# Optimization experiments

Measured on AMD Instinct MI355X. Metric: run time of the kernel, lower is better.

The kernel has to match this reference:

```python
import jax, jax.numpy as jnp
import numpy as np

N_NODES = 50000
N_EDGES = 1_600_000
IN_C, HID_C, OUT_C = 512, 256, 50
ALPHA = 0.1
NUM_LAYERS = 10


def setup_inputs() -> dict:
    key = jax.random.key(0)
    ks = jax.random.split(key, 8)
    x = jax.random.normal(ks[0], (N_NODES, IN_C), dtype=jnp.float32)
    edge_row = jax.random.randint(ks[1], (N_EDGES,), 0, N_NODES, dtype=jnp.int32)
    edge_col = jax.random.randint(ks[2], (N_EDGES,), 0, N_NODES, dtype=jnp.int32)
    edge_weight = jax.random.uniform(ks[3], (N_EDGES,), dtype=jnp.float32)
    s1 = 1.0 / np.sqrt(IN_C)
    s2 = 1.0 / np.sqrt(HID_C)
    W1 = jax.random.uniform(ks[4], (IN_C, HID_C), minval=-s1, maxval=s1, dtype=jnp.float32)
    b1 = jax.random.uniform(ks[5], (HID_C,), minval=-s1, maxval=s1, dtype=jnp.float32)
    W2 = jax.random.uniform(ks[6], (HID_C, OUT_C), minval=-s2, maxval=s2, dtype=jnp.float32)
    b2 = jax.random.uniform(ks[7], (OUT_C,), minval=-s2, maxval=s2, dtype=jnp.float32)
    return {"x": x, "edge_row": edge_row, "edge_col": edge_col,
            "edge_weight": edge_weight, "W1": W1, "b1": b1, "W2": W2, "b2": b2}


def reference(x, edge_row, edge_col, edge_weight, W1, b1, W2, b2):
    # MLP: Linear -> ReLU -> Linear (dropout inactive in eval, no batch norm)
    h = jax.nn.relu(x @ W1 + b1)          # [N, HID_C]
    h = h @ W2 + b2                        # [N, OUT_C]
    x0 = h

    def spmm(v):
        # out[i] = sum_{e: row[e]==i} w[e] * v[col[e]]
        msgs = v[edge_col] * edge_weight[:, None]   # [E, OUT_C]
        return jax.ops.segment_sum(msgs, edge_row, num_segments=N_NODES)

    def step(h, _):
        h = spmm(h) * (1.0 - ALPHA) + ALPHA * x0
        return h, None

    h, _ = jax.lax.scan(step, h, None, length=NUM_LAYERS)
    return jax.nn.log_softmax(h, axis=1)
```

## Files before the change

kernel.cpp:

```cpp
#include <hip/hip_runtime.h>
#include <cstddef>
#include <cstdint>
#include <math.h>

#define N_NODES 50000
#define N_EDGES 1600000
#define IN_C 512
#define HID_C 256
#define OUT_C 50
#define PAD_C 64
#define NUM_LAYERS 10
#define NBUCK 98
#define BSHIFT 9
#define BCAP 20480
#define PHB_CHUNK 8192
#define PHB_BLOCKS 196

typedef __attribute__((ext_vector_type(8))) short short8;
typedef __attribute__((ext_vector_type(4))) float floatx4;

__device__ inline unsigned short f2bf(float f) {
    unsigned int u = __float_as_uint(f);
    u += 0x7fffu + ((u >> 16) & 1u);
    return (unsigned short)(u >> 16);
}

__device__ inline unsigned cvtpk(float lo, float hi) {
    unsigned r;
    asm("v_cvt_pk_bf16_f32 %0, %1, %2" : "=v"(r) : "v"(lo), "v"(hi));
    return r;
}

__device__ inline short8 pack_bf16x8(float4 lo, float4 hi) {
    union { unsigned u[4]; short8 s; } r;
    r.u[0] = cvtpk(lo.x, lo.y);
    r.u[1] = cvtpk(lo.z, lo.w);
    r.u[2] = cvtpk(hi.x, hi.y);
    r.u[3] = cvtpk(hi.z, hi.w);
    return r.s;
}

#define ASYNC16(g, l)                                                     \
    __builtin_amdgcn_global_load_lds(                                     \
        (const __attribute__((address_space(1))) void*)(g),               \
        (__attribute__((address_space(3))) void*)(l), 16, 0, 0)

__global__ __launch_bounds__(256) void transpose_w1(const float* __restrict__ W1,
                                                    unsigned short* __restrict__ Wt) {
    __shared__ float tile[32][33];
    int bx = blockIdx.x;
    int by = blockIdx.y;
    int tx = threadIdx.x & 31, ty = threadIdx.x >> 5;
#pragma unroll
    for (int i = 0; i < 32; i += 8)
        tile[ty + i][tx] = W1[(bx * 32 + ty + i) * HID_C + by * 32 + tx];
    __syncthreads();
#pragma unroll
    for (int i = 0; i < 32; i += 8)
        Wt[(size_t)(by * 32 + ty + i) * IN_C + bx * 32 + tx] = f2bf(tile[tx][ty + i]);
}

__global__ void pad_w2(const float* __restrict__ W2, const float* __restrict__ b2,
                       unsigned short* __restrict__ Wpt, float* __restrict__ bp) {
    int idx = blockIdx.x * blockDim.x + threadIdx.x;
    if (idx < PAD_C * HID_C) {
        int n = idx >> 8, k = idx & 255;
        float v = (n < OUT_C) ? W2[k * OUT_C + n] : 0.f;
        Wpt[idx] = f2bf(v);
    }
    if (idx < PAD_C) bp[idx] = (idx < OUT_C) ? b2[idx] : 0.f;
}

__global__ __launch_bounds__(256) void gemm1_fused(const float* __restrict__ A,
                                                   const unsigned short* __restrict__ Wt,
                                                   const float* __restrict__ b1,
                                                   const unsigned short* __restrict__ Wpt,
                                                   const float* __restrict__ bp,
                                                   float* __restrict__ h0f,
                                                   unsigned short* __restrict__ h0b) {
    __shared__ __align__(16) char smem[33792];
    unsigned short* Bs0 = (unsigned short*)smem;
    unsigned short* Bs1 = (unsigned short*)(smem + 16384);
    unsigned short* Hs  = (unsigned short*)smem;
    const int HS_LD = 264;

    const int tid  = threadIdx.x;
    const int wave = tid >> 6, lane = tid & 63;
    const int quad = lane >> 4, l16 = lane & 15;
    const int m0 = blockIdx.x * 64;
    const int wm = (wave >> 1) * 32;
    const int wn = (wave & 1) * 128;

    floatx4 acc[2][8];
#pragma unroll
    for (int i = 0; i < 2; ++i)
#pragma unroll
        for (int j = 0; j < 8; ++j) acc[i][j] = (floatx4){0.f, 0.f, 0.f, 0.f};

    int r0 = m0 + wm + l16;
    int r1 = r0 + 16;
    if (r0 >= N_NODES) r0 = N_NODES - 1;
    if (r1 >= N_NODES) r1 = N_NODES - 1;
    const float* a0 = A + (size_t)r0 * IN_C + (quad << 3);
    const float* a1 = A + (size_t)r1 * IN_C + (quad << 3);

    auto stageB = [&](unsigned short* Bs_, int k0) {
#pragma unroll
        for (int j = 0; j < 4; ++j) {
            const unsigned short* src = Wt + (size_t)tid * IN_C + k0 + (j << 3);
            ASYNC16(src, Bs_ + (j << 11) + (tid << 3));
        }
    };

    float4 pa[4];
    auto loadA = [&](int k0) {
        pa[0] = *(const float4*)(a0 + k0);
        pa[1] = *(const float4*)(a0 + k0 + 4);
        pa[2] = *(const float4*)(a1 + k0);
        pa[3] = *(const float4*)(a1 + k0 + 4);
    };

    auto compute = [&](const unsigned short* Bs_, short8 af0, short8 af1) {
#pragma unroll
        for (int nt = 0; nt < 8; ++nt) {
            short8 bf = *(const short8*)&Bs_[(quad << 11) + ((wn + nt * 16 + l16) << 3)];
            acc[0][nt] = __builtin_amdgcn_mfma_f32_16x16x32_bf16(af0, bf, acc[0][nt], 0, 0, 0);
            acc[1][nt] = __builtin_amdgcn_mfma_f32_16x16x32_bf16(af1, bf, acc[1][nt], 0, 0, 0);
        }
    };

    stageB(Bs0, 0);
    loadA(0);
    __syncthreads();

    for (int kp = 0; kp < 8; ++kp) {
        const int k0 = kp * 64;
        stageB(Bs1, k0 + 32);
        {
            short8 af0 = pack_bf16x8(pa[0], pa[1]);
            short8 af1 = pack_bf16x8(pa[2], pa[3]);
            loadA(k0 + 32);
            compute(Bs0, af0, af1);
        }
        __syncthreads();
        if (kp < 7) stageB(Bs0, k0 + 64);
        {
            short8 af0 = pack_bf16x8(pa[0], pa[1]);
            short8 af1 = pack_bf16x8(pa[2], pa[3]);
            if (kp < 7) loadA(k0 + 64);
            compute(Bs1, af0, af1);
        }
        __syncthreads();
    }

#pragma unroll
    for (int nt = 0; nt < 8; ++nt) {
        int n = wn + nt * 16 + l16;
        float bn = b1[n];
#pragma unroll
        for (int mt = 0; mt < 2; ++mt)
#pragma unroll
            for (int r = 0; r < 4; ++r) {
                float v = acc[mt][nt][r] + bn;
                v = v > 0.f ? v : 0.f;
                Hs[(wm + mt * 16 + quad * 4 + r) * HS_LD + n] = f2bf(v);
            }
    }
    __syncthreads();

    floatx4 acc2[4];
#pragma unroll
    for (int nt = 0; nt < 4; ++nt) acc2[nt] = (floatx4){0.f, 0.f, 0.f, 0.f};
    const int hrow = (wave << 4) + l16;
#pragma unroll
    for (int k2 = 0; k2 < 8; ++k2) {
        short8 haf = *(const short8*)&Hs[hrow * HS_LD + (k2 << 5) + (quad << 3)];
#pragma unroll
        for (int nt = 0; nt < 4; ++nt) {
            short8 bf = *(const short8*)&Wpt[(size_t)((nt << 4) + l16) * HID_C + (k2 << 5) + (quad << 3)];
            acc2[nt] = __builtin_amdgcn_mfma_f32_16x16x32_bf16(haf, bf, acc2[nt], 0, 0, 0);
        }
    }
#pragma unroll
    for (int nt = 0; nt < 4; ++nt) {
        int c = (nt << 4) + l16;
        float bn = bp[c];
#pragma unroll
        for (int r = 0; r < 4; ++r) {
            int row = m0 + (wave << 4) + (quad << 2) + r;
            if (row < N_NODES) {
                float v = acc2[nt][r] + bn;
                h0f[(size_t)row * PAD_C + c] = v;
                h0b[(size_t)row * PAD_C + c] = f2bf(v);
            }
        }
    }
}

__global__ __launch_bounds__(256) void bucket_scatter(const int* __restrict__ erow,
                                                      const int* __restrict__ ecol,
                                                      const float* __restrict__ ew,
                                                      int* __restrict__ bfill,
                                                      uint2* __restrict__ buckets) {
    __shared__ int lcnt[NBUCK];
    __shared__ int lbase[NBUCK];
    const int t = threadIdx.x;
    for (int b = t; b < NBUCK; b += 256) lcnt[b] = 0;
    __syncthreads();
    const int e0 = blockIdx.x * PHB_CHUNK;
    const int e1 = min(e0 + PHB_CHUNK, N_EDGES);
    for (int e = e0 + t; e < e1; e += 256)
        atomicAdd(&lcnt[erow[e] >> BSHIFT], 1);
    __syncthreads();
    for (int b = t; b < NBUCK; b += 256) {
        lbase[b] = atomicAdd(&bfill[b], lcnt[b]);
        lcnt[b] = 0;
    }
    __syncthreads();
    for (int e = e0 + t; e < e1; e += 256) {
        int r = erow[e];
        int b = r >> BSHIFT;
        int o = atomicAdd(&lcnt[b], 1);
        int idx = lbase[b] + o;
        if (idx < BCAP) {
            unsigned packed = ((unsigned)(r - (b << BSHIFT)) << 17) | (unsigned)ecol[e];
            buckets[(size_t)b * BCAP + idx] = make_uint2(packed, __float_as_uint(ew[e]));
        }
    }
}

__global__ __launch_bounds__(128) void bucket_scan(const int* __restrict__ bfill,
                                                   int* __restrict__ bbase,
                                                   int* __restrict__ rowptr) {
    __shared__ int sd[128];
    int t = threadIdx.x;
    int v = (t < NBUCK) ? min(bfill[t], BCAP) : 0;
    sd[t] = v;
    __syncthreads();
    for (int off = 1; off < 128; off <<= 1) {
        int x = (t >= off) ? sd[t - off] : 0;
        __syncthreads();
        sd[t] += x;
        __syncthreads();
    }
    if (t < NBUCK) bbase[t] = sd[t] - v;
    if (t == NBUCK - 1) {
        bbase[NBUCK] = sd[t];
        rowptr[N_NODES] = sd[t];
    }
}

__global__ __launch_bounds__(256) void bucket_csr(const uint2* __restrict__ buckets,
                                                  const int* __restrict__ bfill,
                                                  const int* __restrict__ bbase,
                                                  int* __restrict__ rowptr,
                                                  uint2* __restrict__ edges) {
    __shared__ int hist[512];
    __shared__ int excl[512];
    __shared__ int psum[256];
    const int b = blockIdx.x;
    const int t = threadIdx.x;
    const int n = min(bfill[b], BCAP);
    const uint2* bk = buckets + (size_t)b * BCAP;

    hist[t] = 0; hist[t + 256] = 0;
    __syncthreads();
    for (int i = t; i < n; i += 256)
        atomicAdd(&hist[bk[i].x >> 17], 1);
    __syncthreads();
    int a0 = hist[2 * t], a1 = hist[2 * t + 1];
    psum[t] = a0 + a1;
    __syncthreads();
    for (int off = 1; off < 256; off <<= 1) {
        int x = (t >= off) ? psum[t - off] : 0;
        __syncthreads();
        psum[t] += x;
        __syncthreads();
    }
    int pe = psum[t] - (a0 + a1);
    excl[2 * t] = pe;
    excl[2 * t + 1] = pe + a0;
    __syncthreads();
    const int base = bbase[b];
#pragma unroll
    for (int k = 0; k < 2; ++k) {
        int lr = t + k * 256;
        int r = (b << BSHIFT) + lr;
        if (r < N_NODES) rowptr[r] = base + excl[lr];
    }
    hist[t] = 0; hist[t + 256] = 0;
    __syncthreads();
    for (int i = t; i < n; i += 256) {
        uint2 ed = bk[i];
        int lr = ed.x >> 17;
        int pos = base + excl[lr] + atomicAdd(&hist[lr], 1);
        edges[pos] = make_uint2(ed.x & 0x1FFFFu, ed.y);
    }
}

__device__ inline void edge_fma(float* acc, float wgt, uint4 hv) {
    acc[0] = fmaf(wgt, __uint_as_float(hv.x << 16),         acc[0]);
    acc[1] = fmaf(wgt, __uint_as_float(hv.x & 0xffff0000u), acc[1]);
    acc[2] = fmaf(wgt, __uint_as_float(hv.y << 16),         acc[2]);
    acc[3] = fmaf(wgt, __uint_as_float(hv.y & 0xffff0000u), acc[3]);
    acc[4] = fmaf(wgt, __uint_as_float(hv.z << 16),         acc[4]);
    acc[5] = fmaf(wgt, __uint_as_float(hv.z & 0xffff0000u), acc[5]);
    acc[6] = fmaf(wgt, __uint_as_float(hv.w << 16),         acc[6]);
    acc[7] = fmaf(wgt, __uint_as_float(hv.w & 0xffff0000u), acc[7]);
}

template <bool LAST>
__global__ __launch_bounds__(256) void prop8(const int* __restrict__ rowptr,
                                             const uint2* __restrict__ edges,
                                             const unsigned short* __restrict__ hin,
                                             const float* __restrict__ h0f,
                                             unsigned short* __restrict__ hout_b,
                                             float* __restrict__ out_f) {
    int wid = (blockIdx.x * blockDim.x + threadIdx.x) >> 6;
    if (wid >= N_NODES) return;
    int lane = threadIdx.x & 63;
    int slot = lane >> 3;
    int lc   = lane & 7;
    int s = rowptr[wid], e = rowptr[wid + 1];

    float acc0[8], acc1[8];
#pragma unroll
    for (int k = 0; k < 8; ++k) { acc0[k] = 0.f; acc1[k] = 0.f; }

    int i = s;
    for (; i + 32 <= e; i += 32) {
        uint2 cw0 = edges[i + slot];
        uint2 cw1 = edges[i + 8 + slot];
        uint2 cw2 = edges[i + 16 + slot];
        uint2 cw3 = edges[i + 24 + slot];
        uint4 hv0 = *(const uint4*)((const char*)hin + ((size_t)cw0.x << 7) + lc * 16);
        uint4 hv1 = *(const uint4*)((const char*)hin + ((size_t)cw1.x << 7) + lc * 16);
        uint4 hv2 = *(const uint4*)((const char*)hin + ((size_t)cw2.x << 7) + lc * 16);
        uint4 hv3 = *(const uint4*)((const char*)hin + ((size_t)cw3.x << 7) + lc * 16);
        edge_fma(acc0, __uint_as_float(cw0.y), hv0);
        edge_fma(acc1, __uint_as_float(cw1.y), hv1);
        edge_fma(acc0, __uint_as_float(cw2.y), hv2);
        edge_fma(acc1, __uint_as_float(cw3.y), hv3);
    }
    for (; i + 16 <= e; i += 16) {
        uint2 cw0 = edges[i + slot];
        uint2 cw1 = edges[i + 8 + slot];
        uint4 hv0 = *(const uint4*)((const char*)hin + ((size_t)cw0.x << 7) + lc * 16);
        uint4 hv1 = *(const uint4*)((const char*)hin + ((size_t)cw1.x << 7) + lc * 16);
        edge_fma(acc0, __uint_as_float(cw0.y), hv0);
        edge_fma(acc1, __uint_as_float(cw1.y), hv1);
    }
    for (; i < e; i += 8) {
        int idx = i + slot;
        uint2 cw = (idx < e) ? edges[idx] : make_uint2(0u, 0u);
        float wgt = (idx < e) ? __uint_as_float(cw.y) : 0.f;
        uint4 hv = *(const uint4*)((const char*)hin + ((size_t)cw.x << 7) + lc * 16);
        edge_fma(acc0, wgt, hv);
    }

    float r[8];
#pragma unroll
    for (int k = 0; k < 8; ++k) {
        float v = acc0[k] + acc1[k];
        v += __shfl_xor(v, 8, 64);
        v += __shfl_xor(v, 16, 64);
        v += __shfl_xor(v, 32, 64);
        r[k] = v;
    }

    size_t off = (size_t)wid * PAD_C + lc * 8;
    float4 h0a = *(const float4*)(h0f + off);
    float4 h0b4 = *(const float4*)(h0f + off + 4);
    r[0] = 0.9f * r[0] + 0.1f * h0a.x;  r[1] = 0.9f * r[1] + 0.1f * h0a.y;
    r[2] = 0.9f * r[2] + 0.1f * h0a.z;  r[3] = 0.9f * r[3] + 0.1f * h0a.w;
    r[4] = 0.9f * r[4] + 0.1f * h0b4.x; r[5] = 0.9f * r[5] + 0.1f * h0b4.y;
    r[6] = 0.9f * r[6] + 0.1f * h0b4.z; r[7] = 0.9f * r[7] + 0.1f * h0b4.w;

    if (!LAST) {
        if (slot == 0) {
            uint4 u;
            u.x = ((unsigned)f2bf(r[1]) << 16) | f2bf(r[0]);
            u.y = ((unsigned)f2bf(r[3]) << 16) | f2bf(r[2]);
            u.z = ((unsigned)f2bf(r[5]) << 16) | f2bf(r[4]);
            u.w = ((unsigned)f2bf(r[7]) << 16) | f2bf(r[6]);
            *(uint4*)((char*)hout_b + ((size_t)wid << 7) + lc * 16) = u;
        }
    } else {
        int ch0 = lc * 8;
        float m = -INFINITY;
#pragma unroll
        for (int k = 0; k < 8; ++k) if (ch0 + k < OUT_C) m = fmaxf(m, r[k]);
        m = fmaxf(m, __shfl_xor(m, 1, 64));
        m = fmaxf(m, __shfl_xor(m, 2, 64));
        m = fmaxf(m, __shfl_xor(m, 4, 64));
        float ss = 0.f;
#pragma unroll
        for (int k = 0; k < 8; ++k) if (ch0 + k < OUT_C) ss += __expf(r[k] - m);
        ss += __shfl_xor(ss, 1, 64);
        ss += __shfl_xor(ss, 2, 64);
        ss += __shfl_xor(ss, 4, 64);
        float lse = __logf(ss);
        if (slot == 0) {
#pragma unroll
            for (int k = 0; k < 8; ++k)
                if (ch0 + k < OUT_C)
                    out_f[(size_t)wid * OUT_C + ch0 + k] = (r[k] - m) - lse;
        }
    }
}

extern "C" void kernel_launch(void* const* d_in, const int* in_sizes, int n_in,
                              void* d_out, int out_size, void* d_ws, size_t ws_size,
                              hipStream_t stream) {
    const float* x    = (const float*)d_in[0];
    const int*   erow = (const int*)d_in[1];
    const int*   ecol = (const int*)d_in[2];
    const float* ew   = (const float*)d_in[3];
    const float* W1   = (const float*)d_in[4];
    const float* b1   = (const float*)d_in[5];
    const float* W2   = (const float*)d_in[6];
    const float* b2   = (const float*)d_in[7];
    float* out = (float*)d_out;

    char* p = (char*)d_ws;
    auto alloc = [&](size_t bytes) {
        char* r = p;
        p += (bytes + 255) & ~(size_t)255;
        return r;
    };
    char*  scratch = alloc((size_t)NBUCK * BCAP * 8);
    float* h0f    = (float*)alloc((size_t)N_NODES * PAD_C * 4);
    unsigned short* h0b = (unsigned short*)alloc((size_t)N_NODES * PAD_C * 2);
    uint2* edges  = (uint2*)alloc((size_t)N_EDGES * 8);
    int*   rowptr = (int*)alloc((size_t)(N_NODES + 1) * 4);
    int*   bfill  = (int*)alloc((size_t)NBUCK * 4);
    int*   bbase  = (int*)alloc((size_t)(NBUCK + 1) * 4);
    float* bp     = (float*)alloc((size_t)PAD_C * 4);
    unsigned short* Wt  = (unsigned short*)alloc((size_t)HID_C * IN_C * 2);
    unsigned short* Wpt = (unsigned short*)alloc((size_t)PAD_C * HID_C * 2);
    uint2* buckets = (uint2*)scratch;
    unsigned short* ha = (unsigned short*)scratch;
    unsigned short* hb = (unsigned short*)(scratch + (size_t)N_NODES * PAD_C * 2);

    hipMemsetAsync(bfill, 0, (size_t)NBUCK * 4, stream);

    bucket_scatter<<<PHB_BLOCKS, 256, 0, stream>>>(erow, ecol, ew, bfill, buckets);
    bucket_scan<<<1, 128, 0, stream>>>(bfill, bbase, rowptr);
    bucket_csr<<<NBUCK, 256, 0, stream>>>(buckets, bfill, bbase, rowptr, edges);

    transpose_w1<<<dim3(IN_C / 32, HID_C / 32), 256, 0, stream>>>(W1, Wt);
    pad_w2<<<(PAD_C * HID_C + 255) / 256, 256, 0, stream>>>(W2, b2, Wpt, bp);
    gemm1_fused<<<(N_NODES + 63) / 64, 256, 0, stream>>>(x, Wt, b1, Wpt, bp, h0f, h0b);

    const int prop_blocks = (N_NODES * 64 + 255) / 256;
    const unsigned short* cur = h0b;
    unsigned short* nxt = ha;
    for (int l = 0; l < NUM_LAYERS - 1; ++l) {
        prop8<false><<<prop_blocks, 256, 0, stream>>>(rowptr, edges, cur, h0f,
                                                      nxt, nullptr);
        const unsigned short* t = nxt;
        nxt = (nxt == ha) ? hb : ha;
        cur = t;
    }
    prop8<true><<<prop_blocks, 256, 0, stream>>>(rowptr, edges, cur, h0f,
                                                 nullptr, out);
}
```

Baseline: 644.5 us.

## Triple-buffer A and B tiles in LDS via async loads for gemm1

The first GEMM now stages both the fp32 A tile, with an XOR swizzle, and the bf16 W1 tile into LDS using async global-to-LDS loads. It uses a three-stage ring buffer with explicit vmcnt waits and barriers, replacing the earlier scheme of register-prefetched A and double-buffered B. The aim is to keep more memory traffic in flight and hide load latency behind the MFMAs. In exchange, LDS use per block grows from about 33KB to 72KB, which may reduce occupancy, and correctness depends on the hand-set waitcnt values.

```diff
diff --git a/kernel.cpp b/kernel.cpp
--- a/kernel.cpp
+++ b/kernel.cpp
@@ -45,6 +45,10 @@
         (const __attribute__((address_space(1))) void*)(g),               \
         (__attribute__((address_space(3))) void*)(l), 16, 0, 0)
 
+#define WAITCNT6() asm volatile("s_waitcnt vmcnt(6)" ::: "memory")
+#define WAITCNT0() asm volatile("s_waitcnt vmcnt(0)" ::: "memory")
+#define SBAR()     __builtin_amdgcn_s_barrier()
+
 __global__ __launch_bounds__(256) void transpose_w1(const float* __restrict__ W1,
                                                     unsigned short* __restrict__ Wt) {
     __shared__ float tile[32][33];
@@ -78,10 +82,14 @@
                                                    const float* __restrict__ bp,
                                                    float* __restrict__ h0f,
                                                    unsigned short* __restrict__ h0b) {
-    __shared__ __align__(16) char smem[33792];
-    unsigned short* Bs0 = (unsigned short*)smem;
-    unsigned short* Bs1 = (unsigned short*)(smem + 16384);
-    unsigned short* Hs  = (unsigned short*)smem;
+    __shared__ __align__(16) char smem[73728];
+    float*          Ab[3] = {(float*)smem,
+                             (float*)(smem + 24576),
+                             (float*)(smem + 49152)};
+    unsigned short* Bb[3] = {(unsigned short*)(smem + 8192),
+                             (unsigned short*)(smem + 32768),
+                             (unsigned short*)(smem + 57344)};
+    unsigned short* Hs = (unsigned short*)smem;
     const int HS_LD = 264;
 
     const int tid  = threadIdx.x;
@@ -97,61 +105,60 @@
 #pragma unroll
         for (int j = 0; j < 8; ++j) acc[i][j] = (floatx4){0.f, 0.f, 0.f, 0.f};
 
-    int r0 = m0 + wm + l16;
-    int r1 = r0 + 16;
-    if (r0 >= N_NODES) r0 = N_NODES - 1;
-    if (r1 >= N_NODES) r1 = N_NODES - 1;
-    const float* a0 = A + (size_t)r0 * IN_C + (quad << 3);
-    const float* a1 = A + (size_t)r1 * IN_C + (quad << 3);
-
-    auto stageB = [&](unsigned short* Bs_, int k0) {
+    const int ar = (tid >> 3), ac = tid & 7;
+    auto stage = [&](int bi, int ks) {
+        const int k0 = ks << 5;
+#pragma unroll
+        for (int j = 0; j < 2; ++j) {
+            int slot = tid + j * 256;
+            int r = slot >> 3, c = slot & 7;
+            int gr = m0 + r;
+            if (gr >= N_NODES) gr = N_NODES - 1;
+            const float* src = A + (size_t)gr * IN_C + k0 + ((c ^ (r & 7)) << 2);
+            ASYNC16(src, Ab[bi] + (slot << 2));
+        }
 #pragma unroll
         for (int j = 0; j < 4; ++j) {
             const unsigned short* src = Wt + (size_t)tid * IN_C + k0 + (j << 3);
-            ASYNC16(src, Bs_ + (j << 11) + (tid << 3));
+            ASYNC16(src, Bb[bi] + (j << 11) + (tid << 3));
         }
     };
 
-    float4 pa[4];
-    auto loadA = [&](int k0) {
-        pa[0] = *(const float4*)(a0 + k0);
-        pa[1] = *(const float4*)(a0 + k0 + 4);
-        pa[2] = *(const float4*)(a1 + k0);
-        pa[3] = *(const float4*)(a1 + k0 + 4);
+    auto compute = [&](int bi) {
+        const float* As_ = Ab[bi];
+        const unsigned short* Bs_ = Bb[bi];
+        short8 bfr[8], afr[2];
+#pragma unroll
+        for (int nt = 0; nt < 8; ++nt)
+            bfr[nt] = *(const short8*)&Bs_[(quad << 11) + ((wn + nt * 16 + l16) << 3)];
+#pragma unroll
+        for (int mt = 0; mt < 2; ++mt) {
+            int r  = wm + mt * 16 + l16;
+            int rx = r & 7;
+            float4 lo = *(const float4*)&As_[(r << 5) + (((2 * quad)     ^ rx) << 2)];
+            float4 hi = *(const float4*)&As_[(r << 5) + (((2 * quad + 1) ^ rx) << 2)];
+            afr[mt] = pack_bf16x8(lo, hi);
+        }
+#pragma unroll
+        for (int mt = 0; mt < 2; ++mt)
+#pragma unroll
+            for (int nt = 0; nt < 8; ++nt)
+                acc[mt][nt] = __builtin_amdgcn_mfma_f32_16x16x32_bf16(afr[mt], bfr[nt],
+                                                                      acc[mt][nt], 0, 0, 0);
     };
 
-    auto compute = [&](const unsigned short* Bs_, short8 af0, short8 af1) {
-#pragma unroll
-        for (int nt = 0; nt < 8; ++nt) {
-            short8 bf = *(const short8*)&Bs_[(quad << 11) + ((wn + nt * 16 + l16) << 3)];
-            acc[0][nt] = __builtin_amdgcn_mfma_f32_16x16x32_bf16(af0, bf, acc[0][nt], 0, 0, 0);
-            acc[1][nt] = __builtin_amdgcn_mfma_f32_16x16x32_bf16(af1, bf, acc[1][nt], 0, 0, 0);
-        }
-    };
-
-    stageB(Bs0, 0);
-    loadA(0);
-    __syncthreads();
-
-    for (int kp = 0; kp < 8; ++kp) {
-        const int k0 = kp * 64;
-        stageB(Bs1, k0 + 32);
-        {
-            short8 af0 = pack_bf16x8(pa[0], pa[1]);
-            short8 af1 = pack_bf16x8(pa[2], pa[3]);
-            loadA(k0 + 32);
-            compute(Bs0, af0, af1);
-        }
-        __syncthreads();
-        if (kp < 7) stageB(Bs0, k0 + 64);
-        {
-            short8 af0 = pack_bf16x8(pa[0], pa[1]);
-            short8 af1 = pack_bf16x8(pa[2], pa[3]);
-            if (kp < 7) loadA(k0 + 64);
-            compute(Bs1, af0, af1);
-        }
-        __syncthreads();
-    }
+    stage(0, 0);
+    stage(1, 1);
+#pragma unroll
+    for (int ks = 0; ks < 14; ++ks) {
+        WAITCNT6();
+        SBAR();
+        stage((ks + 2) % 3, ks + 2);
+        compute(ks % 3);
+    }
+    WAITCNT6(); SBAR(); compute(2);
+    WAITCNT0(); SBAR(); compute(0);
+    __syncthreads();
 
 #pragma unroll
     for (int nt = 0; nt < 8; ++nt) {
```

Measured after the change: 624.6 us. -3.1%, faster.
